# Kernel optimization log

Measured on AMD Instinct MI355X. Metric: run time of the kernel, lower is better.

## Reference

```python
import jax, jax.numpy as jnp
import numpy as np

N_NODES = 100000
N_EDGES = 1600000
IN_DIM = 128
HID = 128
OUT_DIM = 64
EPS = 1e-8


def setup_inputs() -> dict:
    key = jax.random.key(0)
    ks = jax.random.split(key, 10)
    x = jax.random.normal(ks[0], (N_NODES, IN_DIM), dtype=jnp.float32)
    edge_index = jax.random.randint(ks[1], (2, N_EDGES), 0, N_NODES, dtype=jnp.int64)
    edge_attr = jax.random.uniform(ks[2], (N_EDGES, 4), dtype=jnp.float32)
    s1 = 1.0 / np.sqrt(IN_DIM)
    s2 = 1.0 / np.sqrt(HID)
    sr = 1.0 / np.sqrt(2 * HID)
    W1 = jax.random.normal(ks[3], (HID, IN_DIM), dtype=jnp.float32) * s1
    b1 = jnp.zeros((HID,), dtype=jnp.float32)
    W2 = jax.random.normal(ks[4], (HID, HID), dtype=jnp.float32) * s2
    b2 = jnp.zeros((HID,), dtype=jnp.float32)
    Wr = jax.random.normal(ks[5], (OUT_DIM, 2 * HID), dtype=jnp.float32) * sr
    br = jnp.zeros((OUT_DIM,), dtype=jnp.float32)
    return {"x": x, "edge_index": edge_index, "edge_attr": edge_attr,
            "W1": W1, "b1": b1, "W2": W2, "b2": b2, "Wr": Wr, "br": br}


def _edge_weight_from_attr_auto(edge_attr):
    # mean over features, min-max normalize, invert, clamp >= 0
    m = edge_attr.mean(axis=-1)                      # [E]
    m_min, m_max = m.min(), m.max()
    m_norm = (m - m_min) / (m_max - m_min + EPS)
    w = jnp.where(m_max - m_min > EPS, 1.0 - m_norm, jnp.ones_like(m))
    return jnp.clip(w, 0.0)


def reference(x, edge_index, edge_attr, W1, b1, W2, b2, Wr, br):
    N = x.shape[0]
    row, col = edge_index[0], edge_index[1]          # source -> target
    ew = _edge_weight_from_attr_auto(edge_attr)      # [E]
    # GCN normalization with self-loops (self-loop weight = 1.0)
    deg = jax.ops.segment_sum(ew, col, num_segments=N) + 1.0   # [N]
    dis = jax.lax.rsqrt(deg)                         # deg >= 1
    norm = dis[row] * ew * dis[col]                  # [E]

    def gcn(h, W, b):
        hW = h @ W.T                                 # [N, d_out]
        agg = jax.ops.segment_sum(norm[:, None] * hW[row], col, num_segments=N)
        # self-loop contribution: dis[i] * 1.0 * dis[i] * hW[i]
        return agg + (dis * dis)[:, None] * hW + b

    # dropout in eval mode -> identity
    h1 = jax.nn.relu(gcn(x, W1, b1))                 # [N, HID]
    h2 = jax.nn.relu(gcn(h1, W2, b2))                # [N, HID]
    hcat = jnp.concatenate([h1, h2], axis=-1)        # [N, 2*HID] (JK concat)
    return hcat @ Wr.T + br                          # residue-level [N, OUT_DIM]
```

## Files before the change

### kernel.cpp

```cpp
#include <hip/hip_runtime.h>

#define NN 100000
#define NE 1600000
#define HID 128
#define ODIM 64
#define NBK 196
#define BSHIFT 9
#define BINB 200
#define CVTB 8
#define GEMMB 782
#define CHUNK 8000
#define BITER 8
#define BINCAP 12288
#define SMAX 8588
#define LMAX 2148

typedef unsigned int u32;
typedef unsigned short u16;
typedef __bf16 bf16x8 __attribute__((ext_vector_type(8)));
typedef float f32x4 __attribute__((ext_vector_type(4)));
typedef float f32x2 __attribute__((ext_vector_type(2)));

__device__ __forceinline__ float bf_lo(u32 p){ return __uint_as_float(p << 16); }
__device__ __forceinline__ float bf_hi(u32 p){ return __uint_as_float(p & 0xffff0000u); }
__device__ __forceinline__ u16 f2bf(float f){
  u32 u = __float_as_uint(f);
  u += 0x7fffu + ((u >> 16) & 1u);
  return (u16)(u >> 16);
}
__device__ __forceinline__ bf16x8 ld8bf(const u16* p){ return *(const bf16x8*)p; }
__device__ __forceinline__ bf16x8 cvt8(const float* p){
  union { bf16x8 v; u16 s[8]; } r;
#pragma unroll
  for (int i = 0; i < 8; i++) r.s[i] = f2bf(p[i]);
  return r.v;
}

__device__ __forceinline__ void wparams(const u32* minmax, float* A, float* B){
  u32 mnq = 32767u - minmax[0];
  u32 mxq = minmax[1];
  u32 rngq = mxq - mnq;
  float inv = rngq ? 1.f / ((float)rngq * (1.f / 32767.f) + 1e-8f) : 0.f;
  *A = 1.f + (float)mnq * (1.f / 32767.f) * inv;
  *B = inv * (1.f / 32767.f);
}

__global__ __launch_bounds__(1024, 8) void k_front(
    const float* __restrict__ eattr, const int* __restrict__ erow,
    const int* __restrict__ ecol, u32* __restrict__ bcur,
    uint2* __restrict__ bin8, u32* __restrict__ minmax,
    const float* __restrict__ x, const float* __restrict__ W1,
    const float* __restrict__ W2, const float* __restrict__ Wr,
    u16* __restrict__ W2b, u16* __restrict__ Wrb, u16* __restrict__ graw){
  int tid = threadIdx.x;
  int bid = blockIdx.x;
  if (bid >= BINB + CVTB){
    int gblk = bid - BINB - CVTB;
    int wv = tid >> 6, lane = tid & 63;
    int mg = wv >> 2, ng = wv & 3;
    int m0 = gblk * 128 + mg * 32;
    int m = lane & 15, q = lane >> 4;
    const float* a0f = x + (size_t)min(m0 + m, NN - 1) * HID;
    const float* a1f = x + (size_t)min(m0 + 16 + m, NN - 1) * HID;
    const float* brow0 = W1 + (size_t)(ng * 16 + m) * HID;
    const float* brow1 = brow0 + (size_t)64 * HID;
    f32x4 acc00 = {0.f,0.f,0.f,0.f}, acc01 = {0.f,0.f,0.f,0.f};
    f32x4 acc10 = {0.f,0.f,0.f,0.f}, acc11 = {0.f,0.f,0.f,0.f};
#pragma unroll
    for (int kb = 0; kb < HID; kb += 32){
      bf16x8 af0 = cvt8(a0f + kb + q * 8);
      bf16x8 af1 = cvt8(a1f + kb + q * 8);
      bf16x8 bf0 = cvt8(brow0 + kb + q * 8);
      bf16x8 bf1 = cvt8(brow1 + kb + q * 8);
      acc00 = __builtin_amdgcn_mfma_f32_16x16x32_bf16(af0, bf0, acc00, 0, 0, 0);
      acc01 = __builtin_amdgcn_mfma_f32_16x16x32_bf16(af0, bf1, acc01, 0, 0, 0);
      acc10 = __builtin_amdgcn_mfma_f32_16x16x32_bf16(af1, bf0, acc10, 0, 0, 0);
      acc11 = __builtin_amdgcn_mfma_f32_16x16x32_bf16(af1, bf1, acc11, 0, 0, 0);
    }
#pragma unroll
    for (int r = 0; r < 4; r++){
      int row0 = m0 + q * 4 + r, row1 = m0 + 16 + q * 4 + r;
      if (row0 < NN){
        u16* c0 = graw + (size_t)row0 * HID + ng * 16 + m;
        c0[0]  = f2bf(acc00[r]);
        c0[64] = f2bf(acc01[r]);
      }
      if (row1 < NN){
        u16* c1 = graw + (size_t)row1 * HID + ng * 16 + m;
        c1[0]  = f2bf(acc10[r]);
        c1[64] = f2bf(acc11[r]);
      }
    }
    return;
  }
  if (bid >= BINB){
    int i = (bid - BINB) * 1024 + tid;
    const float* src; u16* dst; int off;
    if (i < 4096){ src = W2; dst = W2b; off = i; }
    else { src = Wr; dst = Wrb; off = i - 4096; }
    float4 v = ((const float4*)src)[off];
    uint2 o;
    o.x = (u32)f2bf(v.x) | ((u32)f2bf(v.y) << 16);
    o.y = (u32)f2bf(v.z) | ((u32)f2bf(v.w) << 16);
    ((uint2*)dst)[off] = o;
    return;
  }
  __shared__ u32 lcnt[8 * NBK], wof[8 * NBK];
  __shared__ u32 lofs[NBK], gb[NBK];
  __shared__ u32 wtot[4];
  __shared__ u16 lmap[LMAX];
  __shared__ u32 stageA[SMAX];
  __shared__ u16 stageM[SMAX];
  __shared__ u32 Tt;
  __shared__ u32 sMn[16], sMx[16];
  for (int t = tid; t < 8 * NBK; t += 1024) lcnt[t] = 0;
  __syncthreads();
  int base = bid * CHUNK;
  int wv = tid >> 6, lane = tid & 63;
  int grp = tid >> 7;
  u32 pk[BITER];
#pragma unroll
  for (int it = 0; it < BITER; it++){
    int idx = it * 1024 + tid;
    u32 p = 0xFFFFFFFFu;
    if (idx < CHUNK){
      int c = ecol[base + idx];
      if ((u32)c < NN){
        u32 b = (u32)c >> BSHIFT;
        u32 r = atomicAdd(&lcnt[grp * NBK + b], 1u);
        p = (b << 22) | (((u32)c & 511u) << 13) | r;
      }
    }
    pk[it] = p;
  }
  __syncthreads();
  u32 na = 0;
  if (tid < NBK){
    u32 run = 0;
#pragma unroll
    for (int g = 0; g < 8; g++){
      wof[g * NBK + tid] = run;
      run += lcnt[g * NBK + tid];
    }
    na = (run + 3u) & ~3u;
    lofs[tid] = run;
  }
  u32 incl = na;
  if (tid < 256){
    for (int off = 1; off < 64; off <<= 1){
      u32 t = (u32)__shfl_up((int)incl, off);
      if (lane >= off) incl += t;
    }
    if (lane == 63) wtot[wv] = incl;
  }
  __syncthreads();
  if (tid < 256){
    u32 pre = 0;
#pragma unroll
    for (int k = 0; k < 4; k++) pre += (k < wv) ? wtot[k] : 0u;
    u32 ex = pre + incl - na;
    if (tid == 255) Tt = pre + incl;
    if (tid < NBK){
      u32 n = lofs[tid];
      lofs[tid] = ex;
      u32 g = 0x80000000u;
      if (na){
        u32 gl = atomicAdd(&bcur[tid], na);
        if (gl + na <= BINCAP) g = (u32)tid * BINCAP + gl;
      }
      gb[tid] = g;
      for (u32 l = ex >> 2; l < (ex + na) >> 2; l++) lmap[l] = (u16)tid;
      for (u32 k = n; k < na; k++){ stageA[ex + k] = 0xFFFFFFFFu; stageM[ex + k] = 0; }
    }
  }
  __syncthreads();
  u32 lmn = 0, lmx = 0;
#pragma unroll
  for (int it = 0; it < BITER; it++){
    int idx = it * 1024 + tid;
    if (idx >= CHUNK) continue;
    int e = base + idx;
    float4 a = ((const float4*)eattr)[e];
    float m = 0.25f * (a.x + a.y + a.z + a.w);
    u32 mq = (u32)(m * 32767.f + 0.5f);
    lmn = max(lmn, 32767u - mq); lmx = max(lmx, mq);
    u32 p = pk[it];
    if (p == 0xFFFFFFFFu) continue;
    u32 s = (u32)erow[e]; if (s >= NN) s = 0;
    u32 b = p >> 22, d = (p >> 13) & 511u, r = p & 8191u;
    u32 slot = lofs[b] + wof[grp * NBK + b] + r;
    stageA[slot] = s | (d << 17);
    stageM[slot] = (u16)mq;
  }
  __syncthreads();
  u32 T = Tt;
  for (u32 i = tid; i < T; i += 1024){
    u32 b = lmap[i >> 2];
    u32 g = gb[b];
    if (g != 0x80000000u){
      uint2 rec; rec.x = stageA[i]; rec.y = (u32)stageM[i];
      bin8[g + (i - lofs[b])] = rec;
    }
  }
  for (int off = 32; off; off >>= 1){
    lmn = max(lmn, (u32)__shfl_xor((int)lmn, off));
    lmx = max(lmx, (u32)__shfl_xor((int)lmx, off));
  }
  if (lane == 0){ sMn[wv] = lmn; sMx[wv] = lmx; }
  __syncthreads();
  if (tid == 0){
    u32 mn = 0, mx = 0;
#pragma unroll
    for (int k = 0; k < 16; k++){ mn = max(mn, sMn[k]); mx = max(mx, sMx[k]); }
    atomicMax(&minmax[0], mn);
    atomicMax(&minmax[1], mx);
  }
}

__global__ __launch_bounds__(1024) void k_scatter(
    const u32* __restrict__ bcur, const uint2* __restrict__ bin8,
    const u32* __restrict__ minmax, u32* __restrict__ csr,
    u32* __restrict__ meta, float* __restrict__ dis){
  __shared__ u32 cnt4[4 * 512], sum4[4 * 512];
  __shared__ u32 curL[512];
  __shared__ u32 wtot[8];
  int b = blockIdx.x, tid = threadIdx.x;
  int grp = tid >> 8;
  int bb = b * BINCAP;
  int nrec = (int)min(bcur[b], (u32)BINCAP);
  for (int t = tid; t < 4 * 512; t += 1024){ cnt4[t] = 0; sum4[t] = 0; }
  __syncthreads();
  for (int i = tid; i < nrec; i += 1024){
    uint2 r = bin8[bb + i];
    if (r.x == 0xFFFFFFFFu) continue;
    u32 d = (r.x >> 17) & 511u;
    atomicAdd(&cnt4[grp * 512 + d], 1u);
    atomicAdd(&sum4[grp * 512 + d], r.y);
  }
  __syncthreads();
  float A, B; wparams(minmax, &A, &B);
  int wid = tid >> 6, lane = tid & 63;
  u32 v = 0, sm = 0, incl = 0;
  if (tid < 512){
    v  = cnt4[tid] + cnt4[512 + tid] + cnt4[1024 + tid] + cnt4[1536 + tid];
    sm = sum4[tid] + sum4[512 + tid] + sum4[1024 + tid] + sum4[1536 + tid];
    incl = v;
  }
  for (int off = 1; off < 64; off <<= 1){
    u32 t = (u32)__shfl_up((int)incl, off);
    if (lane >= off) incl += t;
  }
  if (tid < 512 && lane == 63) wtot[wid] = incl;
  __syncthreads();
  if (tid < 512){
    u32 pre = 0;
#pragma unroll
    for (int k = 0; k < 8; k++) pre += (k < wid) ? wtot[k] : 0u;
    u32 ex = pre + incl - v;
    curL[tid] = (u32)bb + ex;
    int node = (b << BSHIFT) + tid;
    if (node < NN){
      meta[node] = ((u32)bb + ex) | (v << 22);
      float sw = A * (float)v - B * (float)sm;
      dis[node] = rsqrtf(1.f + sw);
    }
  }
  __syncthreads();
  for (int i = tid; i < nrec; i += 1024){
    uint2 r = bin8[bb + i];
    if (r.x == 0xFFFFFFFFu) continue;
    u32 d = (r.x >> 17) & 511u;
    u32 pos = atomicAdd(&curL[d], 1u);
    csr[pos] = (r.x & 0x1FFFFu) | (r.y << 17);
  }
}

__global__ __launch_bounds__(256) void k_gemm128(
    const u16* __restrict__ Ab, const u16* __restrict__ Bt,
    const float* __restrict__ dis, u16* __restrict__ G){
  int wave = threadIdx.x >> 6, lane = threadIdx.x & 63;
  int m0 = blockIdx.x * 32;
  int m = lane & 15, q = lane >> 4;
  const u16* a0b = Ab + (size_t)(m0 + m) * HID;
  const u16* a1b = a0b + (size_t)16 * HID;
  const u16* brow0 = Bt + (size_t)(wave * 16 + m) * HID;
  const u16* brow1 = brow0 + (size_t)64 * HID;
  f32x4 acc00 = {0.f,0.f,0.f,0.f}, acc01 = {0.f,0.f,0.f,0.f};
  f32x4 acc10 = {0.f,0.f,0.f,0.f}, acc11 = {0.f,0.f,0.f,0.f};
#pragma unroll
  for (int kb = 0; kb < HID; kb += 32){
    bf16x8 af0 = ld8bf(a0b + kb + q * 8);
    bf16x8 af1 = ld8bf(a1b + kb + q * 8);
    bf16x8 bf0 = ld8bf(brow0 + kb + q * 8);
    bf16x8 bf1 = ld8bf(brow1 + kb + q * 8);
    acc00 = __builtin_amdgcn_mfma_f32_16x16x32_bf16(af0, bf0, acc00, 0, 0, 0);
    acc01 = __builtin_amdgcn_mfma_f32_16x16x32_bf16(af0, bf1, acc01, 0, 0, 0);
    acc10 = __builtin_amdgcn_mfma_f32_16x16x32_bf16(af1, bf0, acc10, 0, 0, 0);
    acc11 = __builtin_amdgcn_mfma_f32_16x16x32_bf16(af1, bf1, acc11, 0, 0, 0);
  }
  u16* crow0 = G + (size_t)(m0 + q * 4) * HID + wave * 16 + m;
  u16* crow1 = crow0 + (size_t)16 * HID;
#pragma unroll
  for (int r = 0; r < 4; r++){
    float d0 = dis[m0 + q * 4 + r];
    float d1 = dis[m0 + 16 + q * 4 + r];
    crow0[(size_t)r * HID]      = f2bf(acc00[r] * d0);
    crow0[(size_t)r * HID + 64] = f2bf(acc01[r] * d0);
    crow1[(size_t)r * HID]      = f2bf(acc10[r] * d1);
    crow1[(size_t)r * HID + 64] = f2bf(acc11[r] * d1);
  }
}

__global__ __launch_bounds__(256) void k_aggregate(
    const u32* __restrict__ meta, const u32* __restrict__ csr,
    const float* __restrict__ dis, const u32* __restrict__ minmax,
    const u16* __restrict__ g, const float* __restrict__ bias,
    u16* __restrict__ hout){
  int node = __builtin_amdgcn_readfirstlane(
      (int)(blockIdx.x * 4 + (threadIdx.x >> 6)));
  int lane = threadIdx.x & 63;
  const u32* gp = (const u32*)g;
  u32 sv = gp[((size_t)node << 6) + lane];
  u32 mw = meta[node];
  float di = dis[node];
  float A, B; wparams(minmax, &A, &B);
  u32 s = mw & 0x3FFFFFu;
  int c = (int)(mw >> 22);
  const u32* cp = csr + s;
  f32x2 acc = {0.f, 0.f};
  int j = 0;
  for (; j + 16 <= c; j += 16){
    u32 p[16];
#pragma unroll
    for (int t = 0; t < 16; t++)
      p[t] = __builtin_amdgcn_readfirstlane(cp[j + t]);
    u32 pv[16];
#pragma unroll
    for (int t = 0; t < 16; t++)
      pv[t] = gp[(size_t)(p[t] & 0x1FFFFu) * 64u + lane];
#pragma unroll
    for (int t = 0; t < 16; t++){
      float wf = (A - B * (float)(p[t] >> 17)) * dis[p[t] & 0x1FFFFu];
      f32x2 val = {bf_lo(pv[t]), bf_hi(pv[t])};
      f32x2 w2 = {wf, wf};
      acc += w2 * val;
    }
  }
  for (; j < c; j += 8){
    u32 p[8];
#pragma unroll
    for (int t = 0; t < 8; t++)
      p[t] = __builtin_amdgcn_readfirstlane(cp[j + t]);
    u32 st[8]; float wv[8];
#pragma unroll
    for (int t = 0; t < 8; t++){
      bool ok = (j + t) < c;
      st[t] = ok ? (p[t] & 0x1FFFFu) : 0u;
      wv[t] = ok ? (A - B * (float)(p[t] >> 17)) * dis[st[t]] : 0.f;
    }
    u32 pv[8];
#pragma unroll
    for (int t = 0; t < 8; t++)
      pv[t] = gp[(size_t)st[t] * 64u + lane];
#pragma unroll
    for (int t = 0; t < 8; t++){
      f32x2 val = {bf_lo(pv[t]), bf_hi(pv[t])};
      f32x2 w2 = {wv[t], wv[t]};
      acc += w2 * val;
    }
  }
  float2 bv = ((const float2*)bias)[lane];
  f32x2 selfv = {bf_lo(sv), bf_hi(sv)};
  float o0 = fmaxf((acc.x + di * selfv.x) * di + bv.x, 0.f);
  float o1 = fmaxf((acc.y + di * selfv.y) * di + bv.y, 0.f);
  ((u32*)hout)[((size_t)node << 6) + lane] = (u32)f2bf(o0) | ((u32)f2bf(o1) << 16);
}

__global__ __launch_bounds__(1024) void k_agg_read(
    const u32* __restrict__ meta, const u32* __restrict__ csr,
    const float* __restrict__ dis, const u32* __restrict__ minmax,
    const u16* __restrict__ g, const float* __restrict__ bias,
    const u16* __restrict__ h1, const u16* __restrict__ Wrb,
    const float* __restrict__ br, float* __restrict__ out){
  __shared__ u16 hc[16][264];
  int wv = threadIdx.x >> 6, lane = threadIdx.x & 63;
  int node0 = blockIdx.x * 16;
  int node = __builtin_amdgcn_readfirstlane(node0 + wv);
  const u32* gp = (const u32*)g;
  u32 sv = gp[((size_t)node << 6) + lane];
  u32 mw = meta[node];
  float di = dis[node];
  float A, B; wparams(minmax, &A, &B);
  u32 s = mw & 0x3FFFFFu;
  int c = (int)(mw >> 22);
  const u32* cp = csr + s;
  f32x2 acc = {0.f, 0.f};
  int j = 0;
  for (; j + 16 <= c; j += 16){
    u32 p[16];
#pragma unroll
    for (int t = 0; t < 16; t++)
      p[t] = __builtin_amdgcn_readfirstlane(cp[j + t]);
    u32 pv[16];
#pragma unroll
    for (int t = 0; t < 16; t++)
      pv[t] = gp[(size_t)(p[t] & 0x1FFFFu) * 64u + lane];
#pragma unroll
    for (int t = 0; t < 16; t++){
      float wf = A - B * (float)(p[t] >> 17);
      f32x2 val = {bf_lo(pv[t]), bf_hi(pv[t])};
      f32x2 w2 = {wf, wf};
      acc += w2 * val;
    }
  }
  for (; j < c; j += 8){
    u32 p[8];
#pragma unroll
    for (int t = 0; t < 8; t++)
      p[t] = __builtin_amdgcn_readfirstlane(cp[j + t]);
    u32 st[8]; float wvv[8];
#pragma unroll
    for (int t = 0; t < 8; t++){
      bool ok = (j + t) < c;
      st[t] = ok ? (p[t] & 0x1FFFFu) : 0u;
      wvv[t] = ok ? (A - B * (float)(p[t] >> 17)) : 0.f;
    }
    u32 pv[8];
#pragma unroll
    for (int t = 0; t < 8; t++)
      pv[t] = gp[(size_t)st[t] * 64u + lane];
#pragma unroll
    for (int t = 0; t < 8; t++){
      f32x2 val = {bf_lo(pv[t]), bf_hi(pv[t])};
      f32x2 w2 = {wvv[t], wvv[t]};
      acc += w2 * val;
    }
  }
  float2 bv = ((const float2*)bias)[lane];
  f32x2 selfv = {bf_lo(sv), bf_hi(sv)};
  float o0 = fmaxf((acc.x + selfv.x) * di + bv.x, 0.f);
  float o1 = fmaxf((acc.y + selfv.y) * di + bv.y, 0.f);
  u32 h2pk = (u32)f2bf(o0) | ((u32)f2bf(o1) << 16);
  *(u32*)&hc[wv][2 * lane] = ((const u32*)h1)[((size_t)node << 6) + lane];
  *(u32*)&hc[wv][128 + 2 * lane] = h2pk;
  __syncthreads();
  if (wv < 4){
    int m = lane & 15, q = lane >> 4;
    const u16* b = Wrb + (size_t)(wv * 16 + m) * (2 * HID);
    f32x4 acc4 = {0.f,0.f,0.f,0.f};
#pragma unroll
    for (int kb = 0; kb < 2 * HID; kb += 32){
      bf16x8 af = *(const bf16x8*)&hc[m][kb + q * 8];
      bf16x8 bf = ld8bf(b + kb + q * 8);
      acc4 = __builtin_amdgcn_mfma_f32_16x16x32_bf16(af, bf, acc4, 0, 0, 0);
    }
    float bb = br[wv * 16 + m];
#pragma unroll
    for (int r = 0; r < 4; r++)
      out[(size_t)(node0 + q * 4 + r) * ODIM + wv * 16 + m] = acc4[r] + bb;
  }
}

extern "C" void kernel_launch(void* const* d_in, const int* in_sizes, int n_in,
                              void* d_out, int out_size, void* d_ws, size_t ws_size,
                              hipStream_t stream){
  const float* x     = (const float*)d_in[0];
  const int*   eidx  = (const int*)d_in[1];
  const float* eattr = (const float*)d_in[2];
  const float* W1    = (const float*)d_in[3];
  const float* b1    = (const float*)d_in[4];
  const float* W2    = (const float*)d_in[5];
  const float* b2    = (const float*)d_in[6];
  const float* Wr    = (const float*)d_in[7];
  const float* br    = (const float*)d_in[8];
  const int* erow  = eidx;
  const int* ecol  = eidx + NE;

  char* w = (char*)d_ws;
  auto carve = [&](size_t bytes) -> void* {
    void* p = (void*)w;
    w += (bytes + 255) & ~(size_t)255;
    return p;
  };
  u32* csr       = (u32*)carve((size_t)NBK * BINCAP * 4);
  u32* bcur      = (u32*)carve(1024);
  u32* minmax    = (u32*)carve(256);
  u32* meta      = (u32*)carve((size_t)NN * 4);
  float* dis     = (float*)carve((size_t)NN * 4);
  u16* W2b       = (u16*)carve((size_t)HID * HID * 2);
  u16* Wrb       = (u16*)carve((size_t)ODIM * 2 * HID * 2);
  u16* g         = (u16*)carve((size_t)NN * HID * 2);
  u16* h1        = (u16*)carve((size_t)NN * HID * 2);
  uint2* bin8    = (uint2*)carve((size_t)NBK * BINCAP * 8);

  hipMemsetAsync(bcur, 0, 1280, stream);
  k_front<<<BINB + CVTB + GEMMB, 1024, 0, stream>>>(
      eattr, erow, ecol, bcur, bin8, minmax,
      x, W1, W2, Wr, W2b, Wrb, g);
  k_scatter<<<NBK, 1024, 0, stream>>>(bcur, bin8, minmax, csr, meta, dis);
  k_aggregate<<<NN / 4, 256, 0, stream>>>(meta, csr, dis, minmax, g, b1, h1);
  k_gemm128<<<NN / 32, 256, 0, stream>>>(h1, W2b, dis, g);
  k_agg_read<<<NN / 16, 1024, 0, stream>>>(meta, csr, dis, minmax, g, b2,
                                           h1, Wrb, br, (float*)d_out);
}
```

Measured before the change: 356.3 us.

## Degree-sort nodes within each bucket to balance aggregation waves

k_scatter now runs a per-bucket counting sort of nodes by in-degree and writes a permutation array. Both aggregation kernels take their node from this permutation, so the waves sharing a block get similar edge counts. This aims to cut the time waves spend waiting on the slowest wave, especially at the __syncthreads before the fused readout MFMA in k_agg_read. In exchange it adds extra shared-memory work to the scatter kernel, one extra indirection per wave, and scattered output row writes instead of contiguous ones.

```diff
diff --git a/kernel.cpp b/kernel.cpp
--- a/kernel.cpp
+++ b/kernel.cpp
@@ -220,7 +220,7 @@
 __global__ __launch_bounds__(1024) void k_scatter(
     const u32* __restrict__ bcur, const uint2* __restrict__ bin8,
     const u32* __restrict__ minmax, u32* __restrict__ csr,
-    u32* __restrict__ meta, float* __restrict__ dis){
+    u32* __restrict__ meta, float* __restrict__ dis, u32* __restrict__ perm){
   __shared__ u32 cnt4[4 * 512], sum4[4 * 512];
   __shared__ u32 curL[512];
   __shared__ u32 wtot[8];
@@ -240,6 +240,7 @@
   __syncthreads();
   float A, B; wparams(minmax, &A, &B);
   int wid = tid >> 6, lane = tid & 63;
+  int node = (b << BSHIFT) + tid;
   u32 v = 0, sm = 0, incl = 0;
   if (tid < 512){
     v  = cnt4[tid] + cnt4[512 + tid] + cnt4[1024 + tid] + cnt4[1536 + tid];
@@ -258,12 +259,37 @@
     for (int k = 0; k < 8; k++) pre += (k < wid) ? wtot[k] : 0u;
     u32 ex = pre + incl - v;
     curL[tid] = (u32)bb + ex;
-    int node = (b << BSHIFT) + tid;
     if (node < NN){
       meta[node] = ((u32)bb + ex) | (v << 22);
       float sw = A * (float)v - B * (float)sm;
       dis[node] = rsqrtf(1.f + sw);
     }
+  }
+  __syncthreads();
+  cnt4[tid] = 0;
+  __syncthreads();
+  bool valid = (tid < 512) && (node < NN);
+  u32 dv = min(v, 511u);
+  if (valid) atomicAdd(&cnt4[dv], 1u);
+  __syncthreads();
+  u32 hv = 0, hincl = 0;
+  if (tid < 512){ hv = cnt4[tid]; hincl = hv; }
+  for (int off = 1; off < 64; off <<= 1){
+    u32 t = (u32)__shfl_up((int)hincl, off);
+    if (lane >= off) hincl += t;
+  }
+  if (tid < 512 && lane == 63) wtot[wid] = hincl;
+  __syncthreads();
+  if (tid < 512){
+    u32 pre = 0;
+#pragma unroll
+    for (int k = 0; k < 8; k++) pre += (k < wid) ? wtot[k] : 0u;
+    cnt4[tid] = pre + hincl - hv;
+  }
+  __syncthreads();
+  if (valid){
+    u32 rank = cnt4[dv] + atomicAdd(&cnt4[512 + dv], 1u);
+    perm[(u32)(b << BSHIFT) + rank] = (u32)node;
   }
   __syncthreads();
   for (int i = tid; i < nrec; i += 1024){
@@ -312,12 +338,12 @@
 }
 
 __global__ __launch_bounds__(256) void k_aggregate(
-    const u32* __restrict__ meta, const u32* __restrict__ csr,
-    const float* __restrict__ dis, const u32* __restrict__ minmax,
-    const u16* __restrict__ g, const float* __restrict__ bias,
-    u16* __restrict__ hout){
+    const u32* __restrict__ perm, const u32* __restrict__ meta,
+    const u32* __restrict__ csr, const float* __restrict__ dis,
+    const u32* __restrict__ minmax, const u16* __restrict__ g,
+    const float* __restrict__ bias, u16* __restrict__ hout){
   int node = __builtin_amdgcn_readfirstlane(
-      (int)(blockIdx.x * 4 + (threadIdx.x >> 6)));
+      (int)perm[blockIdx.x * 4 + (threadIdx.x >> 6)]);
   int lane = threadIdx.x & 63;
   const u32* gp = (const u32*)g;
   u32 sv = gp[((size_t)node << 6) + lane];
@@ -377,15 +403,18 @@
 }
 
 __global__ __launch_bounds__(1024) void k_agg_read(
-    const u32* __restrict__ meta, const u32* __restrict__ csr,
-    const float* __restrict__ dis, const u32* __restrict__ minmax,
-    const u16* __restrict__ g, const float* __restrict__ bias,
-    const u16* __restrict__ h1, const u16* __restrict__ Wrb,
-    const float* __restrict__ br, float* __restrict__ out){
+    const u32* __restrict__ perm, const u32* __restrict__ meta,
+    const u32* __restrict__ csr, const float* __restrict__ dis,
+    const u32* __restrict__ minmax, const u16* __restrict__ g,
+    const float* __restrict__ bias, const u16* __restrict__ h1,
+    const u16* __restrict__ Wrb, const float* __restrict__ br,
+    float* __restrict__ out){
   __shared__ u16 hc[16][264];
+  __shared__ u32 nodeIds[16];
   int wv = threadIdx.x >> 6, lane = threadIdx.x & 63;
-  int node0 = blockIdx.x * 16;
-  int node = __builtin_amdgcn_readfirstlane(node0 + wv);
+  int node = __builtin_amdgcn_readfirstlane(
+      (int)perm[blockIdx.x * 16 + wv]);
+  if (lane == 0) nodeIds[wv] = (u32)node;
   const u32* gp = (const u32*)g;
   u32 sv = gp[((size_t)node << 6) + lane];
   u32 mw = meta[node];
@@ -457,7 +486,7 @@
     float bb = br[wv * 16 + m];
 #pragma unroll
     for (int r = 0; r < 4; r++)
-      out[(size_t)(node0 + q * 4 + r) * ODIM + wv * 16 + m] = acc4[r] + bb;
+      out[(size_t)nodeIds[q * 4 + r] * ODIM + wv * 16 + m] = acc4[r] + bb;
   }
 }
 
@@ -487,6 +516,7 @@
   u32* minmax    = (u32*)carve(256);
   u32* meta      = (u32*)carve((size_t)NN * 4);
   float* dis     = (float*)carve((size_t)NN * 4);
+  u32* perm      = (u32*)carve((size_t)NN * 4);
   u16* W2b       = (u16*)carve((size_t)HID * HID * 2);
   u16* Wrb       = (u16*)carve((size_t)ODIM * 2 * HID * 2);
   u16* g         = (u16*)carve((size_t)NN * HID * 2);
@@ -497,9 +527,9 @@
   k_front<<<BINB + CVTB + GEMMB, 1024, 0, stream>>>(
       eattr, erow, ecol, bcur, bin8, minmax,
       x, W1, W2, Wr, W2b, Wrb, g);
-  k_scatter<<<NBK, 1024, 0, stream>>>(bcur, bin8, minmax, csr, meta, dis);
-  k_aggregate<<<NN / 4, 256, 0, stream>>>(meta, csr, dis, minmax, g, b1, h1);
+  k_scatter<<<NBK, 1024, 0, stream>>>(bcur, bin8, minmax, csr, meta, dis, perm);
+  k_aggregate<<<NN / 4, 256, 0, stream>>>(perm, meta, csr, dis, minmax, g, b1, h1);
   k_gemm128<<<NN / 32, 256, 0, stream>>>(h1, W2b, dis, g);
-  k_agg_read<<<NN / 16, 1024, 0, stream>>>(meta, csr, dis, minmax, g, b2,
+  k_agg_read<<<NN / 16, 1024, 0, stream>>>(perm, meta, csr, dis, minmax, g, b2,
                                            h1, Wrb, br, (float*)d_out);
 }
```

After: 375.5 us. 1.05x slower.
